# Kernel tuning notes

Hardware: AMD Instinct MI355X
Metric: run time of the kernel (lower is better)

## Reference

```python
import jax, jax.numpy as jnp
import numpy as np

N_NODES = 200000
N_EDGES = 3200000
N_GRAPHS = 64
IN_DIM, HIDDEN, OUT_DIM = 128, 16, 64


def setup_inputs() -> dict:
    key = jax.random.key(0)
    ks = jax.random.split(key, 5)
    x = jax.random.normal(ks[0], (N_NODES, IN_DIM), dtype=jnp.float32)
    edge_index = jax.random.randint(ks[1], (2, N_EDGES), 0, N_NODES, dtype=jnp.int64)
    batch = jnp.sort(jax.random.randint(ks[2], (N_NODES,), 0, N_GRAPHS, dtype=jnp.int64))
    W1 = jax.random.normal(ks[3], (IN_DIM, HIDDEN), dtype=jnp.float32) * (1.0 / np.sqrt(IN_DIM))
    W2 = jax.random.normal(ks[4], (HIDDEN, OUT_DIM), dtype=jnp.float32) * (1.0 / np.sqrt(HIDDEN))
    b1 = jnp.zeros((HIDDEN,), jnp.float32)
    b2 = jnp.zeros((OUT_DIM,), jnp.float32)
    return {"x": x, "edge_index": edge_index, "batch": batch,
            "W1": W1, "b1": b1, "W2": W2, "b2": b2, "training": 0}


def _gcn_conv(x, W, b, row, col, n_nodes):
    # PyG GCNConv: add-self-loop symmetric normalization, transform then
    # gather-from-row / scatter-add-to-col.  (row, col) already include self-loops.
    h = x @ W                                             # [N, out]
    deg = jnp.zeros((n_nodes,), h.dtype).at[col].add(1.0)  # degree incl. self-loop (>=1)
    dinv = deg ** -0.5
    norm = dinv[row] * dinv[col]                          # [E+N]
    out = jnp.zeros((n_nodes, W.shape[1]), h.dtype).at[col].add(h[row] * norm[:, None])
    return out + b


def reference(x, edge_index, batch, W1, b1, W2, b2, training):
    n = x.shape[0]
    loops = jnp.arange(n, dtype=edge_index.dtype)
    row = jnp.concatenate([edge_index[0], loops])
    col = jnp.concatenate([edge_index[1], loops])
    h = _gcn_conv(x, W1, b1, row, col, n)
    h = jax.nn.relu(h)
    # F.dropout with training=False is identity (reference is deterministic)
    h = _gcn_conv(h, W2, b2, row, col, n)
    # per-graph sum pooling: replaces the Python torch.where loop
    graph_embeds = jax.ops.segment_sum(h, batch, num_segments=N_GRAPHS)
    return graph_embeds
```

## Files before the change

### kernel.cpp

```cpp
#include <hip/hip_runtime.h>


#define TPB 256
#define CHUNK 4096
#define BK_SHIFT 9
#define NPB 512

__device__ __forceinline__ float bf2f(unsigned short u) {
    union { unsigned int i; float f; } v; v.i = ((unsigned int)u) << 16; return v.f;
}
__device__ __forceinline__ unsigned short f2bf(float f) {
    union { float f; unsigned int i; } v; v.f = f;
    unsigned int r = v.i + 0x7fff + ((v.i >> 16) & 1);
    return (unsigned short)(r >> 16);
}

__global__ __launch_bounds__(TPB) void hist_kernel(const int* __restrict__ col,
                                                   int* __restrict__ counts,
                                                   int E, int nblk, int nbuck) {
    __shared__ int hist[512];
    int t = threadIdx.x;
    for (int i = t; i < nbuck; i += TPB) hist[i] = 0;
    __syncthreads();
    int e0 = blockIdx.x * CHUNK;
    for (int i = t; i < CHUNK; i += TPB) {
        int e = e0 + i;
        if (e < E) atomicAdd(&hist[col[e] >> BK_SHIFT], 1);
    }
    __syncthreads();
    for (int i = t; i < nbuck; i += TPB) counts[i * nblk + blockIdx.x] = hist[i];
}

__global__ __launch_bounds__(TPB) void scan1_kernel(const int* __restrict__ in,
                                                    int* __restrict__ out,
                                                    int* __restrict__ bsum, int L) {
    __shared__ int s[TPB];
    int t = threadIdx.x;
    int i = blockIdx.x * TPB + t;
    int d = (i < L) ? in[i] : 0;
    s[t] = d; __syncthreads();
    for (int off = 1; off < TPB; off <<= 1) {
        int v = (t >= off) ? s[t - off] : 0;
        __syncthreads();
        s[t] += v;
        __syncthreads();
    }
    if (i < L) out[i] = s[t] - d;
    if (t == TPB - 1) bsum[blockIdx.x] = s[t];
}

__global__ __launch_bounds__(1024) void scan2_kernel(int* __restrict__ bsum, int nb) {
    __shared__ int s[1024];
    int t = threadIdx.x;
    int i0 = t * 2, i1 = t * 2 + 1;
    int v0 = (i0 < nb) ? bsum[i0] : 0;
    int v1 = (i1 < nb) ? bsum[i1] : 0;
    int pv = v0 + v1;
    s[t] = pv; __syncthreads();
    for (int off = 1; off < 1024; off <<= 1) {
        int u = (t >= off) ? s[t - off] : 0;
        __syncthreads();
        s[t] += u;
        __syncthreads();
    }
    int exc = s[t] - pv;
    if (i0 < nb) bsum[i0] = exc;
    if (i1 < nb) bsum[i1] = exc + v0;
}

__device__ __forceinline__ int cbase_at(const int* counts, const int* bsum, int f) {
    return counts[f] + bsum[f >> 8];
}

#define GEMM_W16(XV, GB)                                                          \
    {                                                                             \
        _Pragma("unroll")                                                         \
        for (int cc = 0; cc < 16; ++cc) {                                         \
            const float4* w4 = (const float4*)&w1s[((GB) * 16 + cc) * 16];        \
            float4 wa = w4[0], wb = w4[1], wc = w4[2], wd = w4[3];                \
            float xc = (XV)[cc];                                                  \
            acc[0]  = fmaf(xc, wa.x, acc[0]);  acc[1]  = fmaf(xc, wa.y, acc[1]);  \
            acc[2]  = fmaf(xc, wa.z, acc[2]);  acc[3]  = fmaf(xc, wa.w, acc[3]);  \
            acc[4]  = fmaf(xc, wb.x, acc[4]);  acc[5]  = fmaf(xc, wb.y, acc[5]);  \
            acc[6]  = fmaf(xc, wb.z, acc[6]);  acc[7]  = fmaf(xc, wb.w, acc[7]);  \
            acc[8]  = fmaf(xc, wc.x, acc[8]);  acc[9]  = fmaf(xc, wc.y, acc[9]);  \
            acc[10] = fmaf(xc, wc.z, acc[10]); acc[11] = fmaf(xc, wc.w, acc[11]); \
            acc[12] = fmaf(xc, wd.x, acc[12]); acc[13] = fmaf(xc, wd.y, acc[13]); \
            acc[14] = fmaf(xc, wd.z, acc[14]); acc[15] = fmaf(xc, wd.w, acc[15]); \
        }                                                                         \
    }

#define XV16(v0, v1, v2, v3)                                          \
    { v0.x, v0.y, v0.z, v0.w, v1.x, v1.y, v1.z, v1.w,                 \
      v2.x, v2.y, v2.z, v2.w, v3.x, v3.y, v3.z, v3.w }

__global__ __launch_bounds__(TPB, 4) void s1c_gemm_kernel(
        const int* __restrict__ row, const int* __restrict__ col,
        const int* __restrict__ counts, const int* __restrict__ bsum,
        int E, int nblk, int nbuck,
        int* __restrict__ bucketed,
        const float* __restrict__ x, const float* __restrict__ W1,
        unsigned short* __restrict__ h1b, int N, int nbg) {
    __shared__ int lhist[512];
    __shared__ int gd[512];
    __shared__ int part[TPB];
    __shared__ unsigned short sidx[CHUNK];
    __shared__ float w1s[128 * 16];
    int b = (int)blockIdx.x, t = threadIdx.x;
    int M = min(nblk, nbg);
    int role, id;
    if (b < 2 * M) { role = b & 1; id = b >> 1; }
    else           { role = (nblk > nbg) ? 0 : 1; id = b - M; }

    if (role == 0) {
        int e0 = id * CHUNK;
        int nE = min(CHUNK, E - e0);
        lhist[t] = 0; lhist[t + TPB] = 0;
        __syncthreads();
        for (int i = t; i < nE; i += TPB)
            atomicAdd(&lhist[col[e0 + i] >> BK_SHIFT], 1);
        __syncthreads();
        int b0i = 2 * t, b1i = 2 * t + 1;
        int c0 = lhist[b0i], c1 = lhist[b1i];
        int s = c0 + c1;
        part[t] = s; __syncthreads();
        for (int off = 1; off < TPB; off <<= 1) {
            int v = (t >= off) ? part[t - off] : 0;
            __syncthreads();
            part[t] += v;
            __syncthreads();
        }
        int o0 = part[t] - s;
        int o1 = o0 + c0;
        lhist[b0i] = o0; lhist[b1i] = o1;
        if (b0i < nbuck) gd[b0i] = cbase_at(counts, bsum, b0i * nblk + id) - o0;
        if (b1i < nbuck) gd[b1i] = cbase_at(counts, bsum, b1i * nblk + id) - o1;
        __syncthreads();
        for (int i = t; i < nE; i += TPB) {
            int bk = col[e0 + i] >> BK_SHIFT;
            int lp = atomicAdd(&lhist[bk], 1);
            sidx[lp] = (unsigned short)i;
        }
        __syncthreads();
        for (int j = t; j < nE; j += TPB) {
            int i = sidx[j];
            int c = col[e0 + i];
            int r = row[e0 + i];
            bucketed[gd[c >> BK_SHIFT] + j] = ((c & (NPB - 1)) << 18) | r;
        }
        return;
    }
    for (int i = t; i < 128 * 16; i += TPB) w1s[i] = W1[i];
    __syncthreads();
    int n = id * TPB + t;
    if (n >= N) return;
    const float4* xr = (const float4*)(x + (size_t)n * 128);
    float acc[16];
#pragma unroll
    for (int k = 0; k < 16; ++k) acc[k] = 0.f;
    float4 p00 = xr[0],  p01 = xr[1],  p02 = xr[2],  p03 = xr[3];
    float4 p10 = xr[4],  p11 = xr[5],  p12 = xr[6],  p13 = xr[7];
    float4 p20 = xr[8],  p21 = xr[9],  p22 = xr[10], p23 = xr[11];
    float4 p30 = xr[12], p31 = xr[13], p32 = xr[14], p33 = xr[15];
    {
        float xv[16] = XV16(p00, p01, p02, p03);
        p00 = xr[16]; p01 = xr[17]; p02 = xr[18]; p03 = xr[19];
        GEMM_W16(xv, 0);
    }
    {
        float xv[16] = XV16(p10, p11, p12, p13);
        p10 = xr[20]; p11 = xr[21]; p12 = xr[22]; p13 = xr[23];
        GEMM_W16(xv, 1);
    }
    {
        float xv[16] = XV16(p20, p21, p22, p23);
        p20 = xr[24]; p21 = xr[25]; p22 = xr[26]; p23 = xr[27];
        GEMM_W16(xv, 2);
    }
    {
        float xv[16] = XV16(p30, p31, p32, p33);
        p30 = xr[28]; p31 = xr[29]; p32 = xr[30]; p33 = xr[31];
        GEMM_W16(xv, 3);
    }
    {
        float xv[16] = XV16(p00, p01, p02, p03);
        GEMM_W16(xv, 4);
    }
    {
        float xv[16] = XV16(p10, p11, p12, p13);
        GEMM_W16(xv, 5);
    }
    {
        float xv[16] = XV16(p20, p21, p22, p23);
        GEMM_W16(xv, 6);
    }
    {
        float xv[16] = XV16(p30, p31, p32, p33);
        GEMM_W16(xv, 7);
    }
    unsigned int u[8];
#pragma unroll
    for (int j = 0; j < 8; ++j)
        u[j] = (unsigned int)f2bf(acc[2 * j]) | ((unsigned int)f2bf(acc[2 * j + 1]) << 16);
    uint4* o = (uint4*)(h1b + (size_t)n * 16);
    o[0] = make_uint4(u[0], u[1], u[2], u[3]);
    o[1] = make_uint4(u[4], u[5], u[6], u[7]);
}

__global__ __launch_bounds__(TPB) void sort_kernel(
        const int* __restrict__ bucketed,
        const int* __restrict__ counts, const int* __restrict__ bsum,
        int E, int nblk, int nbuck,
        int* __restrict__ csr, int* __restrict__ offs, float* __restrict__ dinv,
        const unsigned short* __restrict__ h1b, unsigned short* __restrict__ h1p, int N) {
    __shared__ int lhist[NPB];
    __shared__ int part[TPB];
    __shared__ float sdinv[NPB];
    int bk = blockIdx.x, t = threadIdx.x;
    int n0 = bk << BK_SHIFT;
    int n1 = min(n0 + NPB, N);
    int e0 = cbase_at(counts, bsum, bk * nblk);
    int e1 = (bk + 1 < nbuck) ? cbase_at(counts, bsum, (bk + 1) * nblk) : E;

    lhist[t] = 0; lhist[t + TPB] = 0;
    __syncthreads();
    for (int i = e0 + t; i < e1; i += TPB)
        atomicAdd(&lhist[bucketed[i] >> 18], 1);
    __syncthreads();

    int base = t * 2;
    int c0 = lhist[base], c1 = lhist[base + 1];
    int s = c0 + c1;
    part[t] = s;
    __syncthreads();
    for (int off = 1; off < TPB; off <<= 1) {
        int v = (t >= off) ? part[t - off] : 0;
        __syncthreads();
        part[t] += v;
        __syncthreads();
    }
    int o0 = e0 + part[t] - s;
    int o1 = o0 + c0;
    lhist[base] = o0; lhist[base + 1] = o1;
    sdinv[base]     = rsqrtf((float)c0 + 1.0f);
    sdinv[base + 1] = rsqrtf((float)c1 + 1.0f);
    int n = n0 + base;
    if (n + 0 < N) { offs[n + 0] = o0; dinv[n + 0] = sdinv[base]; }
    if (n + 1 < N) { offs[n + 1] = o1; dinv[n + 1] = sdinv[base + 1]; }
    __syncthreads();

    for (int i = e0 + t; i < e1; i += TPB) {
        int v = bucketed[i];
        int pos = atomicAdd(&lhist[v >> 18], 1);
        csr[pos] = v & 0x3FFFF;
    }
    int nq = (n1 - n0) * 4;
    for (int i = t; i < nq; i += TPB) {
        float dv = sdinv[i >> 2];
        uint2 u = ((const uint2*)h1b)[(size_t)n0 * 4 + i];
        float f0 = bf2f((unsigned short)(u.x & 0xffff));
        float f1 = bf2f((unsigned short)(u.x >> 16));
        float f2 = bf2f((unsigned short)(u.y & 0xffff));
        float f3 = bf2f((unsigned short)(u.y >> 16));
        ((ushort4*)h1p)[(size_t)n0 * 4 + i] =
            make_ushort4(f2bf(f0 * dv), f2bf(f1 * dv), f2bf(f2 * dv), f2bf(f3 * dv));
    }
    if (bk == 0 && t == 0) offs[N] = E;
}

__global__ __launch_bounds__(TPB) void gather1_kernel(const int* __restrict__ csr,
                                                      const int* __restrict__ offs,
                                                      const unsigned short* __restrict__ h1p,
                                                      const float* __restrict__ dinv,
                                                      const float* __restrict__ b1,
                                                      unsigned short* __restrict__ h2p, int N) {
    int t = threadIdx.x;
    int c = blockIdx.x * 16 + (t >> 4);
    int lane = t & 15;
    int half = lane >> 3;
    int kk = lane & 7;
    if (c >= N) return;
    int p0 = offs[c], p1 = offs[c + 1];
    float a0 = 0.f, a1 = 0.f;
    for (int p = p0; p < p1; p += 32) {
        int s_lo = csr[min(p + lane, p1 - 1)];
        int s_hi = csr[min(p + 16 + lane, p1 - 1)];
        int rem = p1 - p;
        unsigned int u[16];
#pragma unroll
        for (int j = 0; j < 8; ++j) {
            int sj = __shfl(s_lo, 2 * j + half, 16);
            u[j] = *(const unsigned int*)&h1p[(size_t)sj * 16 + 2 * kk];
        }
#pragma unroll
        for (int j = 8; j < 16; ++j) {
            int sj = __shfl(s_hi, 2 * j + half - 16, 16);
            u[j] = *(const unsigned int*)&h1p[(size_t)sj * 16 + 2 * kk];
        }
#pragma unroll
        for (int j = 0; j < 16; ++j) {
            bool ok = (2 * j + half) < rem;
            a0 += ok ? bf2f((unsigned short)(u[j] & 0xffff)) : 0.f;
            a1 += ok ? bf2f((unsigned short)(u[j] >> 16)) : 0.f;
        }
    }
    a0 += __shfl_xor(a0, 8, 16);
    a1 += __shfl_xor(a1, 8, 16);
    if (half == 0) {
        float dc = dinv[c];
        unsigned int us = *(const unsigned int*)&h1p[(size_t)c * 16 + 2 * kk];
        float s0 = bf2f((unsigned short)(us & 0xffff));
        float s1 = bf2f((unsigned short)(us >> 16));
        float r0 = fmaf(dc, a0 + s0, b1[2 * kk]);
        float r1 = fmaf(dc, a1 + s1, b1[2 * kk + 1]);
        r0 = dc * fmaxf(r0, 0.f);
        r1 = dc * fmaxf(r1, 0.f);
        unsigned int w = (unsigned int)f2bf(r0) | ((unsigned int)f2bf(r1) << 16);
        *(unsigned int*)&h2p[(size_t)c * 16 + 2 * kk] = w;
    }
}

__global__ __launch_bounds__(TPB) void gather2f_kernel(
        const int* __restrict__ csr, const int* __restrict__ offs,
        const unsigned short* __restrict__ h2p, const float* __restrict__ dinv,
        const float* __restrict__ W2, const float* __restrict__ b2,
        const int* __restrict__ batch, float* __restrict__ out, int N) {
    __shared__ float w2s[16 * 64];
    __shared__ float asT[64 * 17];
    __shared__ float pool[64];
    int t = threadIdx.x;
    for (int i = t; i < 16 * 64; i += TPB) w2s[i] = W2[i];
    if (t < 64) pool[t] = 0.f;

    int n0 = blockIdx.x * 64;
    int nLast = min(n0 + 63, N - 1);
    int g0 = batch[n0];
    bool uniform = (batch[nLast] == g0);

    int grp = t >> 4, lane = t & 15;
    int half = lane >> 3, kk = lane & 7;
#pragma unroll 1
    for (int it = 0; it < 4; ++it) {
        int m = grp * 4 + it;
        int c = n0 + m;
        if (c < N) {
            int p0 = offs[c], p1 = offs[c + 1];
            float a0 = 0.f, a1 = 0.f;
            for (int p = p0; p < p1; p += 32) {
                int s_lo = csr[min(p + lane, p1 - 1)];
                int s_hi = csr[min(p + 16 + lane, p1 - 1)];
                int rem = p1 - p;
                unsigned int u[16];
#pragma unroll
                for (int j = 0; j < 8; ++j) {
                    int sj = __shfl(s_lo, 2 * j + half, 16);
                    u[j] = *(const unsigned int*)&h2p[(size_t)sj * 16 + 2 * kk];
                }
#pragma unroll
                for (int j = 8; j < 16; ++j) {
                    int sj = __shfl(s_hi, 2 * j + half - 16, 16);
                    u[j] = *(const unsigned int*)&h2p[(size_t)sj * 16 + 2 * kk];
                }
#pragma unroll
                for (int j = 0; j < 16; ++j) {
                    bool ok = (2 * j + half) < rem;
                    a0 += ok ? bf2f((unsigned short)(u[j] & 0xffff)) : 0.f;
                    a1 += ok ? bf2f((unsigned short)(u[j] >> 16)) : 0.f;
                }
            }
            a0 += __shfl_xor(a0, 8, 16);
            a1 += __shfl_xor(a1, 8, 16);
            if (half == 0) {
                float dc = dinv[c];
                unsigned int us = *(const unsigned int*)&h2p[(size_t)c * 16 + 2 * kk];
                float s0 = bf2f((unsigned short)(us & 0xffff));
                float s1 = bf2f((unsigned short)(us >> 16));
                asT[m * 17 + 2 * kk]     = dc * (a0 + s0);
                asT[m * 17 + 2 * kk + 1] = dc * (a1 + s1);
            }
        }
    }
    __syncthreads();

    int wave = t >> 6, j = t & 63;
    float w2reg[16];
#pragma unroll
    for (int kx = 0; kx < 16; ++kx) w2reg[kx] = w2s[kx * 64 + j];
    float b2j = b2[j];
    float val = 0.f;
    int g_cur = -1;
#pragma unroll 1
    for (int mi = 0; mi < 16; ++mi) {
        int m = wave * 16 + mi;
        int c = n0 + m;
        if (c >= N) break;
        const float* ar = &asT[m * 17];
        float y = b2j;
#pragma unroll
        for (int kx = 0; kx < 16; ++kx) y = fmaf(ar[kx], w2reg[kx], y);
        if (uniform) {
            val += y;
        } else {
            int g = batch[c];
            if (g != g_cur) {
                if (g_cur >= 0) atomicAdd(&out[(size_t)g_cur * 64 + j], val);
                val = 0.f;
                g_cur = g;
            }
            val += y;
        }
    }
    if (uniform) {
        atomicAdd(&pool[j], val);
        __syncthreads();
        if (t < 64) atomicAdd(&out[(size_t)g0 * 64 + t], pool[t]);
    } else {
        if (g_cur >= 0) atomicAdd(&out[(size_t)g_cur * 64 + j], val);
    }
}

static inline size_t align64(size_t v) { return (v + 63) & ~(size_t)63; }

extern "C" void kernel_launch(void* const* d_in, const int* in_sizes, int n_in,
                              void* d_out, int out_size, void* d_ws, size_t ws_size,
                              hipStream_t stream) {
    const float* x     = (const float*)d_in[0];
    const int*   ei    = (const int*)d_in[1];
    const int*   batch = (const int*)d_in[2];
    const float* W1    = (const float*)d_in[3];
    const float* b1    = (const float*)d_in[4];
    const float* W2    = (const float*)d_in[5];
    const float* b2    = (const float*)d_in[6];

    const int N = in_sizes[0] / 128;
    const int E = in_sizes[1] / 2;
    const int* row = ei;
    const int* col = ei + E;

    const int NBLK  = (E + CHUNK - 1) / CHUNK;
    const int NBUCK = (N + NPB - 1) / NPB;
    const int L     = NBUCK * NBLK;
    const int NBS   = (L + TPB - 1) / TPB;
    const int NBG   = (N + TPB - 1) / TPB;

    char* p = (char*)d_ws;
    int*            counts   = (int*)p;            p += align64((size_t)L * 4);
    int*            bsum     = (int*)p;            p += align64(2048 * 4);
    int*            bucketed = (int*)p;            p += align64((size_t)E * 4);
    int*            csr      = (int*)p;            p += align64((size_t)E * 4);
    int*            offs     = (int*)p;            p += align64((size_t)(N + 1) * 4);
    float*          dinv     = (float*)p;          p += align64((size_t)N * 4);
    unsigned short* h1b      = (unsigned short*)p; p += align64((size_t)N * 16 * 2);
    unsigned short* h1p      = (unsigned short*)p; p += align64((size_t)N * 16 * 2);
    unsigned short* h2p      = (unsigned short*)p; p += align64((size_t)N * 16 * 2);
    float*          out      = (float*)d_out;

    hipMemsetAsync(out, 0, (size_t)out_size * sizeof(float), stream);

    hist_kernel<<<NBLK, TPB, 0, stream>>>(col, counts, E, NBLK, NBUCK);
    scan1_kernel<<<NBS, TPB, 0, stream>>>(counts, counts, bsum, L);
    scan2_kernel<<<1, 1024, 0, stream>>>(bsum, NBS);
    s1c_gemm_kernel<<<NBLK + NBG, TPB, 0, stream>>>(row, col, counts, bsum,
                                                    E, NBLK, NBUCK,
                                                    bucketed, x, W1, h1b, N, NBG);
    sort_kernel<<<NBUCK, TPB, 0, stream>>>(bucketed, counts, bsum, E, NBLK, NBUCK,
                                           csr, offs, dinv, h1b, h1p, N);
    gather1_kernel<<<(N + 15) / 16, TPB, 0, stream>>>(csr, offs, h1p, dinv, b1, h2p, N);
    gather2f_kernel<<<(N + 63) / 64, TPB, 0, stream>>>(csr, offs, h2p, dinv,
                                                       W2, b2, batch, out, N);
}
```

Baseline: 351.8 us.

## Use 16-byte gathers in GCN aggregation and skip recount in bucket scatter

The two gather kernels now have each lane load a full 16-byte half-row (8 bf16 values) per neighbor instead of 4 bytes, with masked accumulation and a wider cross-lane reduction. This cuts the number of memory instructions in the latency-bound neighbor gathers. The bucketing scatter role no longer rebuilds the local histogram with shared atomics: it derives per-bucket counts from the global prefix sums and replaces the block-wide shared-memory scan with a wave-shuffle scan. Shared memory is unioned into one buffer and the occupancy hint is dropped. The cost is more register use and extra shuffle reductions per node.

```diff
diff --git a/kernel.cpp b/kernel.cpp
--- a/kernel.cpp
+++ b/kernel.cpp
@@ -13,6 +13,21 @@
     union { float f; unsigned int i; } v; v.f = f;
     unsigned int r = v.i + 0x7fff + ((v.i >> 16) & 1);
     return (unsigned short)(r >> 16);
+}
+__device__ __forceinline__ void bfacc8(uint4 v, unsigned int m, float* a) {
+    union { unsigned int i; float f; } lo, hi;
+    v.x &= m; v.y &= m; v.z &= m; v.w &= m;
+    lo.i = v.x << 16; hi.i = v.x & 0xffff0000u; a[0] += lo.f; a[1] += hi.f;
+    lo.i = v.y << 16; hi.i = v.y & 0xffff0000u; a[2] += lo.f; a[3] += hi.f;
+    lo.i = v.z << 16; hi.i = v.z & 0xffff0000u; a[4] += lo.f; a[5] += hi.f;
+    lo.i = v.w << 16; hi.i = v.w & 0xffff0000u; a[6] += lo.f; a[7] += hi.f;
+}
+__device__ __forceinline__ void bfunp8(uint4 v, float* a) {
+    union { unsigned int i; float f; } lo, hi;
+    lo.i = v.x << 16; hi.i = v.x & 0xffff0000u; a[0] = lo.f; a[1] = hi.f;
+    lo.i = v.y << 16; hi.i = v.y & 0xffff0000u; a[2] = lo.f; a[3] = hi.f;
+    lo.i = v.z << 16; hi.i = v.z & 0xffff0000u; a[4] = lo.f; a[5] = hi.f;
+    lo.i = v.w << 16; hi.i = v.w & 0xffff0000u; a[6] = lo.f; a[7] = hi.f;
 }
 
 __global__ __launch_bounds__(TPB) void hist_kernel(const int* __restrict__ col,
@@ -94,18 +109,20 @@
     { v0.x, v0.y, v0.z, v0.w, v1.x, v1.y, v1.z, v1.w,                 \
       v2.x, v2.y, v2.z, v2.w, v3.x, v3.y, v3.z, v3.w }
 
-__global__ __launch_bounds__(TPB, 4) void s1c_gemm_kernel(
+__global__ __launch_bounds__(TPB) void s1c_gemm_kernel(
         const int* __restrict__ row, const int* __restrict__ col,
         const int* __restrict__ counts, const int* __restrict__ bsum,
         int E, int nblk, int nbuck,
         int* __restrict__ bucketed,
         const float* __restrict__ x, const float* __restrict__ W1,
         unsigned short* __restrict__ h1b, int N, int nbg) {
-    __shared__ int lhist[512];
-    __shared__ int gd[512];
-    __shared__ int part[TPB];
-    __shared__ unsigned short sidx[CHUNK];
-    __shared__ float w1s[128 * 16];
+    __shared__ __align__(16) char sbuf[2048 + 2048 + 8192 + 64];
+    int* slhist = (int*)sbuf;
+    int* sgd    = (int*)(sbuf + 2048);
+    unsigned short* ssidx = (unsigned short*)(sbuf + 4096);
+    int* swtot  = (int*)(sbuf + 4096 + 8192);
+    float* w1s  = (float*)sbuf;
+
     int b = (int)blockIdx.x, t = threadIdx.x;
     int M = min(nblk, nbg);
     int role, id;
@@ -115,38 +132,50 @@
     if (role == 0) {
         int e0 = id * CHUNK;
         int nE = min(CHUNK, E - e0);
-        lhist[t] = 0; lhist[t + TPB] = 0;
-        __syncthreads();
-        for (int i = t; i < nE; i += TPB)
-            atomicAdd(&lhist[col[e0 + i] >> BK_SHIFT], 1);
-        __syncthreads();
-        int b0i = 2 * t, b1i = 2 * t + 1;
-        int c0 = lhist[b0i], c1 = lhist[b1i];
+        int Ltot = nbuck * nblk;
+        int lane = t & 63, w = t >> 6;
+        int bk0 = 2 * t, bk1 = 2 * t + 1;
+        int cb0 = 0, cb1 = 0, c0 = 0, c1 = 0;
+        if (bk0 < nbuck) {
+            int f = bk0 * nblk + id;
+            cb0 = cbase_at(counts, bsum, f);
+            int nx = (f + 1 < Ltot) ? cbase_at(counts, bsum, f + 1) : E;
+            c0 = nx - cb0;
+        }
+        if (bk1 < nbuck) {
+            int f = bk1 * nblk + id;
+            cb1 = cbase_at(counts, bsum, f);
+            int nx = (f + 1 < Ltot) ? cbase_at(counts, bsum, f + 1) : E;
+            c1 = nx - cb1;
+        }
         int s = c0 + c1;
-        part[t] = s; __syncthreads();
-        for (int off = 1; off < TPB; off <<= 1) {
-            int v = (t >= off) ? part[t - off] : 0;
-            __syncthreads();
-            part[t] += v;
-            __syncthreads();
-        }
-        int o0 = part[t] - s;
+        int v = s;
+#pragma unroll
+        for (int d = 1; d < 64; d <<= 1) {
+            int u2 = __shfl_up(v, d, 64);
+            if (lane >= d) v += u2;
+        }
+        if (lane == 63) swtot[w] = v;
+        __syncthreads();
+        int wbase = 0;
+#pragma unroll
+        for (int i = 0; i < 4; ++i) wbase += (i < w) ? swtot[i] : 0;
+        int o0 = wbase + v - s;
         int o1 = o0 + c0;
-        lhist[b0i] = o0; lhist[b1i] = o1;
-        if (b0i < nbuck) gd[b0i] = cbase_at(counts, bsum, b0i * nblk + id) - o0;
-        if (b1i < nbuck) gd[b1i] = cbase_at(counts, bsum, b1i * nblk + id) - o1;
+        if (bk0 < nbuck) { slhist[bk0] = o0; sgd[bk0] = cb0 - o0; }
+        if (bk1 < nbuck) { slhist[bk1] = o1; sgd[bk1] = cb1 - o1; }
         __syncthreads();
         for (int i = t; i < nE; i += TPB) {
-            int bk = col[e0 + i] >> BK_SHIFT;
-            int lp = atomicAdd(&lhist[bk], 1);
-            sidx[lp] = (unsigned short)i;
+            int c = col[e0 + i];
+            int lp = atomicAdd(&slhist[c >> BK_SHIFT], 1);
+            ssidx[lp] = (unsigned short)i;
         }
         __syncthreads();
         for (int j = t; j < nE; j += TPB) {
-            int i = sidx[j];
+            int i = ssidx[j];
             int c = col[e0 + i];
             int r = row[e0 + i];
-            bucketed[gd[c >> BK_SHIFT] + j] = ((c & (NPB - 1)) << 18) | r;
+            bucketed[sgd[c >> BK_SHIFT] + j] = ((c & (NPB - 1)) << 18) | r;
         }
         return;
     }
@@ -276,47 +305,45 @@
                                                       unsigned short* __restrict__ h2p, int N) {
     int t = threadIdx.x;
     int c = blockIdx.x * 16 + (t >> 4);
-    int lane = t & 15;
-    int half = lane >> 3;
-    int kk = lane & 7;
+    int l = t & 15;
+    int half = l & 1;
+    int sub  = l >> 1;
     if (c >= N) return;
     int p0 = offs[c], p1 = offs[c + 1];
-    float a0 = 0.f, a1 = 0.f;
-    for (int p = p0; p < p1; p += 32) {
-        int s_lo = csr[min(p + lane, p1 - 1)];
-        int s_hi = csr[min(p + 16 + lane, p1 - 1)];
-        int rem = p1 - p;
-        unsigned int u[16];
-#pragma unroll
-        for (int j = 0; j < 8; ++j) {
-            int sj = __shfl(s_lo, 2 * j + half, 16);
-            u[j] = *(const unsigned int*)&h1p[(size_t)sj * 16 + 2 * kk];
-        }
-#pragma unroll
-        for (int j = 8; j < 16; ++j) {
-            int sj = __shfl(s_hi, 2 * j + half - 16, 16);
-            u[j] = *(const unsigned int*)&h1p[(size_t)sj * 16 + 2 * kk];
-        }
-#pragma unroll
-        for (int j = 0; j < 16; ++j) {
-            bool ok = (2 * j + half) < rem;
-            a0 += ok ? bf2f((unsigned short)(u[j] & 0xffff)) : 0.f;
-            a1 += ok ? bf2f((unsigned short)(u[j] >> 16)) : 0.f;
-        }
-    }
-    a0 += __shfl_xor(a0, 8, 16);
-    a1 += __shfl_xor(a1, 8, 16);
-    if (half == 0) {
+    float a[8];
+#pragma unroll
+    for (int k = 0; k < 8; ++k) a[k] = 0.f;
+    for (int p = p0; p < p1; p += 16) {
+        int s16 = csr[min(p + l, p1 - 1)];
+#pragma unroll
+        for (int h = 0; h < 2; ++h) {
+            int e = 8 * h + sub;
+            int src = __shfl(s16, e, 16);
+            unsigned int m = ((p + e) < p1) ? 0xffffffffu : 0u;
+            uint4 v = *(const uint4*)&h1p[(size_t)src * 16 + 8 * half];
+            bfacc8(v, m, a);
+        }
+    }
+#pragma unroll
+    for (int d = 2; d < 16; d <<= 1) {
+#pragma unroll
+        for (int k = 0; k < 8; ++k) a[k] += __shfl_xor(a[k], d, 16);
+    }
+    if (l < 2) {
         float dc = dinv[c];
-        unsigned int us = *(const unsigned int*)&h1p[(size_t)c * 16 + 2 * kk];
-        float s0 = bf2f((unsigned short)(us & 0xffff));
-        float s1 = bf2f((unsigned short)(us >> 16));
-        float r0 = fmaf(dc, a0 + s0, b1[2 * kk]);
-        float r1 = fmaf(dc, a1 + s1, b1[2 * kk + 1]);
-        r0 = dc * fmaxf(r0, 0.f);
-        r1 = dc * fmaxf(r1, 0.f);
-        unsigned int w = (unsigned int)f2bf(r0) | ((unsigned int)f2bf(r1) << 16);
-        *(unsigned int*)&h2p[(size_t)c * 16 + 2 * kk] = w;
+        uint4 sv = *(const uint4*)&h1p[(size_t)c * 16 + 8 * l];
+        float sf[8];
+        bfunp8(sv, sf);
+        unsigned int uo[4];
+#pragma unroll
+        for (int q = 0; q < 4; ++q) {
+            float r0 = fmaf(dc, a[2 * q] + sf[2 * q], b1[8 * l + 2 * q]);
+            float r1 = fmaf(dc, a[2 * q + 1] + sf[2 * q + 1], b1[8 * l + 2 * q + 1]);
+            r0 = dc * fmaxf(r0, 0.f);
+            r1 = dc * fmaxf(r1, 0.f);
+            uo[q] = (unsigned int)f2bf(r0) | ((unsigned int)f2bf(r1) << 16);
+        }
+        *(uint4*)&h2p[(size_t)c * 16 + 8 * l] = make_uint4(uo[0], uo[1], uo[2], uo[3]);
     }
 }
 
@@ -337,46 +364,41 @@
     int g0 = batch[n0];
     bool uniform = (batch[nLast] == g0);
 
-    int grp = t >> 4, lane = t & 15;
-    int half = lane >> 3, kk = lane & 7;
+    int grp = t >> 4, l = t & 15;
+    int half = l & 1, sub = l >> 1;
 #pragma unroll 1
     for (int it = 0; it < 4; ++it) {
         int m = grp * 4 + it;
         int c = n0 + m;
         if (c < N) {
             int p0 = offs[c], p1 = offs[c + 1];
-            float a0 = 0.f, a1 = 0.f;
-            for (int p = p0; p < p1; p += 32) {
-                int s_lo = csr[min(p + lane, p1 - 1)];
-                int s_hi = csr[min(p + 16 + lane, p1 - 1)];
-                int rem = p1 - p;
-                unsigned int u[16];
-#pragma unroll
-                for (int j = 0; j < 8; ++j) {
-                    int sj = __shfl(s_lo, 2 * j + half, 16);
-                    u[j] = *(const unsigned int*)&h2p[(size_t)sj * 16 + 2 * kk];
-                }
-#pragma unroll
-                for (int j = 8; j < 16; ++j) {
-                    int sj = __shfl(s_hi, 2 * j + half - 16, 16);
-                    u[j] = *(const unsigned int*)&h2p[(size_t)sj * 16 + 2 * kk];
-                }
-#pragma unroll
-                for (int j = 0; j < 16; ++j) {
-                    bool ok = (2 * j + half) < rem;
-                    a0 += ok ? bf2f((unsigned short)(u[j] & 0xffff)) : 0.f;
-                    a1 += ok ? bf2f((unsigned short)(u[j] >> 16)) : 0.f;
+            float a[8];
+#pragma unroll
+            for (int k = 0; k < 8; ++k) a[k] = 0.f;
+            for (int p = p0; p < p1; p += 16) {
+                int s16 = csr[min(p + l, p1 - 1)];
+#pragma unroll
+                for (int h = 0; h < 2; ++h) {
+                    int e = 8 * h + sub;
+                    int src = __shfl(s16, e, 16);
+                    unsigned int mm = ((p + e) < p1) ? 0xffffffffu : 0u;
+                    uint4 v = *(const uint4*)&h2p[(size_t)src * 16 + 8 * half];
+                    bfacc8(v, mm, a);
                 }
             }
-            a0 += __shfl_xor(a0, 8, 16);
-            a1 += __shfl_xor(a1, 8, 16);
-            if (half == 0) {
+#pragma unroll
+            for (int d = 2; d < 16; d <<= 1) {
+#pragma unroll
+                for (int k = 0; k < 8; ++k) a[k] += __shfl_xor(a[k], d, 16);
+            }
+            if (l < 2) {
                 float dc = dinv[c];
-                unsigned int us = *(const unsigned int*)&h2p[(size_t)c * 16 + 2 * kk];
-                float s0 = bf2f((unsigned short)(us & 0xffff));
-                float s1 = bf2f((unsigned short)(us >> 16));
-                asT[m * 17 + 2 * kk]     = dc * (a0 + s0);
-                asT[m * 17 + 2 * kk + 1] = dc * (a1 + s1);
+                uint4 sv = *(const uint4*)&h2p[(size_t)c * 16 + 8 * l];
+                float sf[8];
+                bfunp8(sv, sf);
+#pragma unroll
+                for (int k = 0; k < 8; ++k)
+                    asT[m * 17 + 8 * l + k] = dc * (a[k] + sf[k]);
             }
         }
     }
```

Result: no change. 357.1 us (+1.5%).
